# Performance work log

Measured on AMD Instinct MI355X. Metric: run time of the kernel, lower is better.

Reference implementation:

```python
import jax, jax.numpy as jnp
import numpy as np

B, C, H, W = 2, 128, 64, 64
HEADS, DHEAD = 4, 32
K = 7           # kernel_size (dilation = 1)
GROUPS = 32
EPS = 1e-5
DA = HEADS * DHEAD


def setup_inputs() -> dict:
    key = jax.random.key(0)
    ks = jax.random.split(key, 8)
    s = lambda k, sh: jax.random.normal(k, sh, jnp.float32) * 0.02
    return {
        "x": jax.random.normal(ks[0], (B, C, H, W), jnp.float32),
        "gn_weight": jnp.ones((C,), jnp.float32),
        "gn_bias": jnp.zeros((C,), jnp.float32),
        "wq": s(ks[1], (DA, C)), "bq": jnp.zeros((DA,), jnp.float32),
        "wk": s(ks[2], (DA, C)), "bk": jnp.zeros((DA,), jnp.float32),
        "wv": s(ks[3], (DA, C)), "bv": jnp.zeros((DA,), jnp.float32),
        "wo": s(ks[4], (C, DA)), "bo": jnp.zeros((C,), jnp.float32),
        "rpb": s(ks[5], (HEADS, 2 * K - 1, 2 * K - 1)),
    }


def _win_starts(L):
    # NATTEN window start: clamp so the k-window stays in-bounds
    return jnp.clip(jnp.arange(L) - K // 2, 0, L - K)


def _pb_starts(L):
    # NATTEN relative-position-bias start index along one axis
    idx = jnp.arange(L)
    ns = K // 2
    return ns + jnp.maximum(ns - idx, 0) + jnp.minimum(L - idx - 1 - ns, 0)


def reference(x, gn_weight, gn_bias, wq, bq, wk, bk, wv, bv, wo, bo, rpb):
    Bn, Cn, Hn, Wn = x.shape
    # GroupNorm (biased variance, like torch)
    xg = x.reshape(Bn, GROUPS, -1)
    mu = xg.mean(-1, keepdims=True)
    var = xg.var(-1, keepdims=True)
    xg = (xg - mu) * jax.lax.rsqrt(var + EPS)
    xn = xg.reshape(Bn, Cn, Hn, Wn) * gn_weight[:, None, None] + gn_bias[:, None, None]

    def proj(w, b):
        # 1x1 conv == channel matmul; -> (B, heads, H, W, d)
        y = jnp.einsum('bchw,oc->bohw', xn, w) + b[:, None, None]
        return y.reshape(Bn, HEADS, DHEAD, Hn, Wn).transpose(0, 1, 3, 4, 2)

    q = proj(wq, bq) * (DHEAD ** -0.5)
    k = proj(wk, bk)
    v = proj(wv, bv)

    off = jnp.arange(K)
    ih = _win_starts(Hn)[:, None] + off        # (H, K) neighbor rows
    iw = _win_starts(Wn)[:, None] + off        # (W, K) neighbor cols
    # gathered windows: (B, heads, H, W, K, K, d)
    kw = k[:, :, ih[:, None, :, None], iw[None, :, None, :], :]
    vw = v[:, :, ih[:, None, :, None], iw[None, :, None, :], :]

    bh = _pb_starts(Hn)[:, None] + off         # (H, K)
    bw = _pb_starts(Wn)[:, None] + off         # (W, K)
    bias = rpb[:, bh[:, None, :, None], bw[None, :, None, :]]  # (heads, H, W, K, K)

    attn = jnp.einsum('nhpqd,nhpqijd->nhpqij', q, kw) + bias[None]
    attn = jax.nn.softmax(attn.reshape(Bn, HEADS, Hn, Wn, K * K), axis=-1)
    attn = attn.reshape(Bn, HEADS, Hn, Wn, K, K)
    out = jnp.einsum('nhpqij,nhpqijd->nhpqd', attn, vw)  # (B, heads, H, W, d)
    # faithful to the torch code: raw reshape (B,heads,H,W,d)->(B,H,W,heads*d)
    xo = out.reshape(Bn, Hn, Wn, HEADS * DHEAD).transpose(0, 3, 1, 2)
    return jnp.einsum('bchw,oc->bohw', xo, wo) + bo[:, None, None]
```

## Files before the change

### kernel.cpp

```cpp
#include <hip/hip_runtime.h>

#define EPS 1e-5f

typedef short s8v __attribute__((ext_vector_type(8)));
typedef float f4v __attribute__((ext_vector_type(4)));

static __device__ inline short f2bf(float f) {
  return __builtin_bit_cast(short, (__bf16)f);
}

#define OFF_SP    0
#define OFF_S2P   256
#define OFF_WCB   512
#define OFF_BC    (OFF_WCB + 24576)
#define OFF_QB    (OFF_BC + 384)
#define OFF_KB    (OFF_QB + 524288)
#define OFF_VTB   (OFF_KB + 524288)
#define OFF_WOB   (OFF_VTB + 524288)

__global__ __launch_bounds__(256) void kP(
    const float* __restrict__ wq, const float* __restrict__ bq,
    const float* __restrict__ wk, const float* __restrict__ bk,
    const float* __restrict__ wv, const float* __restrict__ bv,
    const float* __restrict__ wo, const float* __restrict__ x,
    short* __restrict__ Wcb, float* __restrict__ bc,
    short* __restrict__ WoB, float* __restrict__ Spart, float* __restrict__ S2part) {
  int blk = blockIdx.x;
  int tid = threadIdx.x;
  if (blk < 64) {
    int t = blk * 256 + tid;
    const float qs = 0.17677669529663687f;
    Wcb[t]         = f2bf(wq[t] * qs);
    Wcb[16384 + t] = f2bf(wk[t]);
    Wcb[32768 + t] = f2bf(wv[t]);
    WoB[t]         = f2bf(wo[t]);
    if (t < 128) {
      bc[t]       = bq[t] * qs;
      bc[128 + t] = bk[t];
      bc[256 + t] = bv[t];
    }
  } else {
    int idx = blk - 64;
    int g = idx >> 2, part = idx & 3;
    const float4* xp = (const float4*)(x + (size_t)g * 16384 + part * 4096);
    float s = 0.f, s2 = 0.f;
    #pragma unroll
    for (int i = 0; i < 4; i++) {
      float4 v = xp[tid + i * 256];
      s  += v.x + v.y + v.z + v.w;
      s2 += v.x*v.x + v.y*v.y + v.z*v.z + v.w*v.w;
    }
    #pragma unroll
    for (int o = 32; o; o >>= 1) {
      s  += __shfl_down(s, o, 64);
      s2 += __shfl_down(s2, o, 64);
    }
    __shared__ float ls[4], ls2[4];
    int wid = tid >> 6, lane = tid & 63;
    if (!lane) { ls[wid] = s; ls2[wid] = s2; }
    __syncthreads();
    if (tid == 0) {
      float S = 0.f, S2 = 0.f;
      #pragma unroll
      for (int i = 0; i < 4; i++) { S += ls[i]; S2 += ls2[i]; }
      Spart[idx]  = S;
      S2part[idx] = S2;
    }
  }
}

__global__ __launch_bounds__(256) void k2_qkv(
    const float* __restrict__ x,
    const float* __restrict__ Spart, const float* __restrict__ S2part,
    const float* __restrict__ gw, const float* __restrict__ gb,
    const short* __restrict__ Wcb, const float* __restrict__ bc,
    short* __restrict__ qb, short* __restrict__ kb, short* __restrict__ vtb) {
  __shared__ short xn[64][136];
  __shared__ short WL[192][136];
  __shared__ float bcs[192];
  __shared__ float sm_s[128], sm_t[128];
  int bid    = blockIdx.x;
  int ptile  = bid >> 1, nslice = bid & 1;
  int b      = ptile >> 6;
  int pbase  = (ptile & 63) * 64;
  int nbase  = nslice * 192;
  int tid    = threadIdx.x;
  int w      = __builtin_amdgcn_readfirstlane(tid >> 6);
  int lane   = tid & 63;

  float va[16], vb[16];
  #pragma unroll
  for (int i = 0; i < 16; i++) {
    int c0 = (w + i * 4) * 2;
    va[i] = x[((size_t)(b * 128 + c0))     * 4096 + pbase + lane];
    vb[i] = x[((size_t)(b * 128 + c0 + 1)) * 4096 + pbase + lane];
  }
  if (tid < 128) {
    int c = tid, gi = (b * 32 + (c >> 2)) * 4;
    float S  = Spart[gi]  + Spart[gi + 1]  + Spart[gi + 2]  + Spart[gi + 3];
    float S2 = S2part[gi] + S2part[gi + 1] + S2part[gi + 2] + S2part[gi + 3];
    float mean = S * (1.f / 16384.f);
    float var  = S2 * (1.f / 16384.f) - mean * mean;
    float sv   = rsqrtf(var + EPS) * gw[c];
    sm_s[c] = sv;
    sm_t[c] = gb[c] - mean * sv;
  }
  #pragma unroll
  for (int i = 0; i < 12; i++) {
    int cc = tid + i * 256;
    int row = cc >> 4, c8 = (cc & 15) * 8;
    *(s8v*)&WL[row][c8] = *(const s8v*)&Wcb[(nbase + row) * 128 + c8];
  }
  if (tid < 192) bcs[tid] = bc[nbase + tid];
  __syncthreads();

  #pragma unroll
  for (int i = 0; i < 16; i++) {
    int c0 = (w + i * 4) * 2;
    ushort e0 = (ushort)f2bf(fmaf(va[i], sm_s[c0],     sm_t[c0]));
    ushort e1 = (ushort)f2bf(fmaf(vb[i], sm_s[c0 + 1], sm_t[c0 + 1]));
    *(uint*)&xn[lane][c0] = ((uint)e1 << 16) | e0;
  }
  __syncthreads();

  int l15 = lane & 15, kh = lane >> 4;
  f4v acc[12];
  #pragma unroll
  for (int nt = 0; nt < 12; nt++) acc[nt] = (f4v){0.f, 0.f, 0.f, 0.f};
  #pragma unroll
  for (int ks = 0; ks < 4; ks++) {
    s8v a = *(s8v*)&xn[w * 16 + l15][ks * 32 + kh * 8];
    #pragma unroll
    for (int nt = 0; nt < 12; nt++) {
      s8v wf = *(s8v*)&WL[nt * 16 + l15][ks * 32 + kh * 8];
      if (nbase + nt * 16 < 256)
        acc[nt] = __builtin_amdgcn_mfma_f32_16x16x32_bf16(wf, a, acc[nt], 0, 0, 0);
      else
        acc[nt] = __builtin_amdgcn_mfma_f32_16x16x32_bf16(a, wf, acc[nt], 0, 0, 0);
    }
  }
  #pragma unroll
  for (int nt = 0; nt < 12; nt++) {
    if (nbase + nt * 16 < 256) {
      int ob  = nt * 16 + kh * 4;
      int o0i = nbase + ob;
      int hd  = (o0i & 127) >> 5, d0 = o0i & 31;
      int bh2 = b * 4 + hd;
      int px  = pbase + w * 16 + l15;
      short* dst = (o0i >> 7) ? kb : qb;
      ushort e0 = (ushort)f2bf(acc[nt][0] + bcs[ob + 0]);
      ushort e1 = (ushort)f2bf(acc[nt][1] + bcs[ob + 1]);
      ushort e2 = (ushort)f2bf(acc[nt][2] + bcs[ob + 2]);
      ushort e3 = (ushort)f2bf(acc[nt][3] + bcs[ob + 3]);
      uint2 pk = make_uint2(((uint)e1 << 16) | e0, ((uint)e3 << 16) | e2);
      *(uint2*)&dst[((size_t)bh2 * 4096 + px) * 32 + d0] = pk;
    } else {
      int o   = nbase + nt * 16 + l15;
      int hd  = (o & 127) >> 5, d = o & 31;
      int bh2 = b * 4 + hd;
      int px0 = pbase + w * 16 + kh * 4;
      float bias = bcs[nt * 16 + l15];
      ushort s0 = (ushort)f2bf(acc[nt][0] + bias);
      ushort s1 = (ushort)f2bf(acc[nt][1] + bias);
      ushort s2 = (ushort)f2bf(acc[nt][2] + bias);
      ushort s3 = (ushort)f2bf(acc[nt][3] + bias);
      uint2 pk2 = make_uint2(((uint)s1 << 16) | s0, ((uint)s3 << 16) | s2);
      *(uint2*)&vtb[((size_t)bh2 * 32 + d) * 4096 + px0] = pk2;
    }
  }
}

__global__ __launch_bounds__(512) void k3_attn_proj(
    const short* __restrict__ qb, const short* __restrict__ kb, const short* __restrict__ vtb,
    const float* __restrict__ rpb, const short* __restrict__ WoB,
    const float* __restrict__ bo, float* __restrict__ out) {
  __shared__ ushort K_s[8][64][32];
  __shared__ ushort VT_s[8][32][68];
  __shared__ ushort P_s[8][16][40];
  __shared__ ushort Wo_s[128][136];
  __shared__ ushort tile_s[2][16][136];
  __shared__ float  rpb_s[176];

  int lb    = blockIdx.x;
  int bh    = lb & 7;
  int chunk = lb >> 3;
  int y0    = chunk * 2;
  int head  = bh & 3, b = bh >> 2;
  int tid   = threadIdx.x;
  int w     = __builtin_amdgcn_readfirstlane(tid >> 6);
  int lane  = tid & 63, l15 = lane & 15, kh = lane >> 4;
  int wsub  = w & 3, rsel = w >> 2;
  int y     = y0 + rsel;
  int ys0   = min(max(y0 - 3, 0), 57);
  int ysoff = min(max(y - 3, 0), 57) - ys0;

  {
    const size_t kbase = (size_t)bh * 4096 * 32;
    #pragma unroll
    for (int i = 0; i < 4; i++) {
      int cc = tid + i * 512;
      int row = cc >> 8, rem = cc & 255;
      int col = rem >> 2, ch8 = (rem & 3) * 8;
      int yr = min(ys0 + row, 63);
      *(s8v*)&K_s[row][col][ch8] = *(const s8v*)&kb[kbase + (size_t)(yr * 64 + col) * 32 + ch8];
    }
  }
  {
    const size_t vbase = (size_t)bh * 32 * 4096;
    #pragma unroll
    for (int i = 0; i < 4; i++) {
      int cc = tid + i * 512;
      int row = cc >> 8, rem = cc & 255;
      int d = rem >> 3, c8 = (rem & 7) * 8;
      int yr = min(ys0 + row, 63);
      *(s8v*)&VT_s[row][d][c8] = *(const s8v*)&vtb[vbase + (size_t)d * 4096 + yr * 64 + c8];
    }
  }
  #pragma unroll
  for (int i = 0; i < 4; i++) {
    int cc = tid + i * 512;
    int row = cc >> 4, c8 = (cc & 15) * 8;
    *(s8v*)&Wo_s[row][c8] = *(const s8v*)&WoB[row * 128 + c8];
  }
  if (tid < 169) rpb_s[tid] = rpb[head * 169 + tid];
  __syncthreads();

  int c0  = wsub * 8 + (wsub >> 1) * 8;
  int xq  = wsub * 16 + l15;
  int xs  = min(max(xq - 3, 0), 57);
  int pbw = 3 + max(3 - xq, 0) + min(60 - xq, 0);
  int pbh = 3 + max(3 - y, 0) + min(60 - y, 0);

  s8v qf = *(const s8v*)&qb[((size_t)bh * 4096 + y * 64 + xq) * 32 + kh * 8];

  int   bidx[8];
  float badd[8];
  #pragma unroll
  for (int j = 0; j < 8; ++j) {
    int cc = (j >> 2) * 16 + kh * 4 + (j & 3);
    int dx = c0 + cc - xs;
    bool valid = (dx >= 0) && (dx < 7);
    bidx[j] = pbw + min(max(dx, 0), 6);
    badd[j] = valid ? 0.f : -1e30f;
  }

  const f4v zero = {0.f, 0.f, 0.f, 0.f};
  f4v o0 = zero, o1 = zero;
  float ssum = 0.f;

  #pragma unroll
  for (int row = 0; row < 7; ++row) {
    int kr = ysoff + row;
    s8v ka0 = *(s8v*)&K_s[kr][c0 + l15][kh * 8];
    s8v ka1 = *(s8v*)&K_s[kr][c0 + 16 + l15][kh * 8];
    f4v lg0 = __builtin_amdgcn_mfma_f32_16x16x32_bf16(ka0, qf, zero, 0, 0, 0);
    f4v lg1 = __builtin_amdgcn_mfma_f32_16x16x32_bf16(ka1, qf, zero, 0, 0, 0);
    int rbase = (pbh + row) * 13;
    float p[8];
    #pragma unroll
    for (int j = 0; j < 4; ++j) {
      p[j]     = __expf(lg0[j] + rpb_s[rbase + bidx[j]]     + badd[j]);
      p[j + 4] = __expf(lg1[j] + rpb_s[rbase + bidx[j + 4]] + badd[j + 4]);
      ssum += p[j] + p[j + 4];
    }
    uint u0 = ((uint)(ushort)f2bf(p[1]) << 16) | (ushort)f2bf(p[0]);
    uint u1 = ((uint)(ushort)f2bf(p[3]) << 16) | (ushort)f2bf(p[2]);
    uint u2 = ((uint)(ushort)f2bf(p[5]) << 16) | (ushort)f2bf(p[4]);
    uint u3 = ((uint)(ushort)f2bf(p[7]) << 16) | (ushort)f2bf(p[6]);
    *(uint2*)&P_s[w][l15][kh * 4]      = make_uint2(u0, u1);
    *(uint2*)&P_s[w][l15][16 + kh * 4] = make_uint2(u2, u3);
    s8v pa  = *(s8v*)&P_s[w][l15][kh * 8];
    s8v vt0 = *(s8v*)&VT_s[kr][l15][c0 + kh * 8];
    s8v vt1 = *(s8v*)&VT_s[kr][16 + l15][c0 + kh * 8];
    o0 = __builtin_amdgcn_mfma_f32_16x16x32_bf16(pa, vt0, o0, 0, 0, 0);
    o1 = __builtin_amdgcn_mfma_f32_16x16x32_bf16(pa, vt1, o1, 0, 0, 0);
  }

  ssum += __shfl_xor(ssum, 16, 64);
  ssum += __shfl_xor(ssum, 32, 64);

  {
    int col = wsub * 4 + kh;
    #pragma unroll
    for (int r = 0; r < 4; ++r) {
      float sq = __builtin_bit_cast(float,
          __builtin_amdgcn_ds_bpermute((kh * 4 + r) << 2, __builtin_bit_cast(int, ssum)));
      float inv = 1.f / sq;
      tile_s[rsel][col][r * 32 + l15]      = (ushort)f2bf(o0[r] * inv);
      tile_s[rsel][col][r * 32 + 16 + l15] = (ushort)f2bf(o1[r] * inv);
    }
  }
  __syncthreads();

  f4v acc2[2];
  acc2[0] = zero; acc2[1] = zero;
  #pragma unroll
  for (int ks = 0; ks < 4; ks++) {
    s8v a = *(s8v*)&tile_s[rsel][l15][ks * 32 + kh * 8];
    #pragma unroll
    for (int nt = 0; nt < 2; nt++) {
      s8v bf = *(s8v*)&Wo_s[wsub * 32 + nt * 16 + l15][ks * 32 + kh * 8];
      acc2[nt] = __builtin_amdgcn_mfma_f32_16x16x32_bf16(a, bf, acc2[nt], 0, 0, 0);
    }
  }
  int pxg = (head * 16 + (y >> 2)) * 64 + ((y & 3) << 4);
  #pragma unroll
  for (int nt = 0; nt < 2; nt++) {
    int o = wsub * 32 + nt * 16 + l15;
    float bias = bo[o];
    float4 val = make_float4(acc2[nt][0] + bias, acc2[nt][1] + bias,
                             acc2[nt][2] + bias, acc2[nt][3] + bias);
    *(float4*)&out[((size_t)b * 128 + o) * 4096 + pxg + kh * 4] = val;
  }
}

extern "C" void kernel_launch(void* const* d_in, const int* in_sizes, int n_in,
                              void* d_out, int out_size, void* d_ws, size_t ws_size,
                              hipStream_t stream) {
  (void)in_sizes; (void)n_in; (void)out_size; (void)ws_size;
  const float* x   = (const float*)d_in[0];
  const float* gw  = (const float*)d_in[1];
  const float* gb  = (const float*)d_in[2];
  const float* wq  = (const float*)d_in[3];
  const float* bq  = (const float*)d_in[4];
  const float* wk  = (const float*)d_in[5];
  const float* bk  = (const float*)d_in[6];
  const float* wv  = (const float*)d_in[7];
  const float* bv  = (const float*)d_in[8];
  const float* wo  = (const float*)d_in[9];
  const float* bo  = (const float*)d_in[10];
  const float* rpb = (const float*)d_in[11];
  float* ws     = (float*)d_ws;
  float* Spart  = ws + OFF_SP;
  float* S2part = ws + OFF_S2P;
  short* Wcb    = (short*)(ws + OFF_WCB);
  float* bc     = ws + OFF_BC;
  short* qb     = (short*)(ws + OFF_QB);
  short* kb     = (short*)(ws + OFF_KB);
  short* vtb    = (short*)(ws + OFF_VTB);
  short* WoB    = (short*)(ws + OFF_WOB);
  float* out    = (float*)d_out;

  hipLaunchKernelGGL(kP, dim3(320), dim3(256), 0, stream,
                     wq, bq, wk, bk, wv, bv, wo, x, Wcb, bc, WoB, Spart, S2part);
  hipLaunchKernelGGL(k2_qkv, dim3(256), dim3(256), 0, stream,
                     x, Spart, S2part, gw, gb, Wcb, bc, qb, kb, vtb);
  hipLaunchKernelGGL(k3_attn_proj, dim3(256), dim3(512), 0, stream,
                     qb, kb, vtb, rpb, WoB, bo, out);
}
```

Before: 26.96 us.

## Split attention kernel into one-row blocks and keep Wo fragments in registers

The attention+projection kernel now uses 512 blocks of 256 threads, each handling a single query row instead of two. This cuts the staged K/V tile from 8 rows to 7 and drops the shared-memory Wo copy: each wave loads its Wo fragments directly into registers. The P buffer is reused as the output tile after an added barrier. All QK logits are computed up front before the softmax/PV loop to give the scheduler more independent MFMA work. Shared memory per block shrinks so more blocks can be resident, at the cost of more register pressure and redundant K/V and Wo loads across blocks.

New measurement: 28.70 us. 6.5% more time.

```diff
diff --git a/kernel.cpp b/kernel.cpp
--- a/kernel.cpp
+++ b/kernel.cpp
@@ -170,68 +170,62 @@
   }
 }
 
-__global__ __launch_bounds__(512) void k3_attn_proj(
+__global__ __launch_bounds__(256, 2) void k3_attn_proj(
     const short* __restrict__ qb, const short* __restrict__ kb, const short* __restrict__ vtb,
     const float* __restrict__ rpb, const short* __restrict__ WoB,
     const float* __restrict__ bo, float* __restrict__ out) {
-  __shared__ ushort K_s[8][64][32];
-  __shared__ ushort VT_s[8][32][68];
-  __shared__ ushort P_s[8][16][40];
-  __shared__ ushort Wo_s[128][136];
-  __shared__ ushort tile_s[2][16][136];
+  __shared__ ushort K_s[7][64][32];
+  __shared__ ushort VT_s[7][32][68];
+  __shared__ ushort PT_s[4][16][36];
   __shared__ float  rpb_s[176];
 
-  int lb    = blockIdx.x;
-  int bh    = lb & 7;
-  int chunk = lb >> 3;
-  int y0    = chunk * 2;
-  int head  = bh & 3, b = bh >> 2;
-  int tid   = threadIdx.x;
-  int w     = __builtin_amdgcn_readfirstlane(tid >> 6);
-  int lane  = tid & 63, l15 = lane & 15, kh = lane >> 4;
-  int wsub  = w & 3, rsel = w >> 2;
-  int y     = y0 + rsel;
-  int ys0   = min(max(y0 - 3, 0), 57);
-  int ysoff = min(max(y - 3, 0), 57) - ys0;
+  int lb   = blockIdx.x;
+  int bh   = lb & 7;
+  int y    = lb >> 3;
+  int head = bh & 3, b = bh >> 2;
+  int tid  = threadIdx.x;
+  int w    = __builtin_amdgcn_readfirstlane(tid >> 6);
+  int lane = tid & 63, l15 = lane & 15, kh = lane >> 4;
+  int ys   = min(max(y - 3, 0), 57);
+
+  int c0  = w * 8 + (w >> 1) * 8;
+  int xq  = w * 16 + l15;
+  s8v wof[2][4];
+  #pragma unroll
+  for (int nt = 0; nt < 2; nt++)
+    #pragma unroll
+    for (int ks = 0; ks < 4; ks++)
+      wof[nt][ks] = *(const s8v*)&WoB[(w * 32 + nt * 16 + l15) * 128 + ks * 32 + kh * 8];
+  s8v qf = *(const s8v*)&qb[((size_t)bh * 4096 + y * 64 + xq) * 32 + kh * 8];
 
   {
     const size_t kbase = (size_t)bh * 4096 * 32;
     #pragma unroll
-    for (int i = 0; i < 4; i++) {
-      int cc = tid + i * 512;
+    for (int i = 0; i < 7; i++) {
+      int cc = tid + i * 256;
       int row = cc >> 8, rem = cc & 255;
       int col = rem >> 2, ch8 = (rem & 3) * 8;
-      int yr = min(ys0 + row, 63);
-      *(s8v*)&K_s[row][col][ch8] = *(const s8v*)&kb[kbase + (size_t)(yr * 64 + col) * 32 + ch8];
+      *(s8v*)&K_s[row][col][ch8] =
+          *(const s8v*)&kb[kbase + (size_t)((ys + row) * 64 + col) * 32 + ch8];
     }
   }
   {
     const size_t vbase = (size_t)bh * 32 * 4096;
     #pragma unroll
-    for (int i = 0; i < 4; i++) {
-      int cc = tid + i * 512;
+    for (int i = 0; i < 7; i++) {
+      int cc = tid + i * 256;
       int row = cc >> 8, rem = cc & 255;
       int d = rem >> 3, c8 = (rem & 7) * 8;
-      int yr = min(ys0 + row, 63);
-      *(s8v*)&VT_s[row][d][c8] = *(const s8v*)&vtb[vbase + (size_t)d * 4096 + yr * 64 + c8];
-    }
-  }
-  #pragma unroll
-  for (int i = 0; i < 4; i++) {
-    int cc = tid + i * 512;
-    int row = cc >> 4, c8 = (cc & 15) * 8;
-    *(s8v*)&Wo_s[row][c8] = *(const s8v*)&WoB[row * 128 + c8];
+      *(s8v*)&VT_s[row][d][c8] =
+          *(const s8v*)&vtb[vbase + (size_t)d * 4096 + (ys + row) * 64 + c8];
+    }
   }
   if (tid < 169) rpb_s[tid] = rpb[head * 169 + tid];
   __syncthreads();
 
-  int c0  = wsub * 8 + (wsub >> 1) * 8;
-  int xq  = wsub * 16 + l15;
   int xs  = min(max(xq - 3, 0), 57);
   int pbw = 3 + max(3 - xq, 0) + min(60 - xq, 0);
   int pbh = 3 + max(3 - y, 0) + min(60 - y, 0);
-
-  s8v qf = *(const s8v*)&qb[((size_t)bh * 4096 + y * 64 + xq) * 32 + kh * 8];
 
   int   bidx[8];
   float badd[8];
@@ -245,33 +239,37 @@
   }
 
   const f4v zero = {0.f, 0.f, 0.f, 0.f};
+
+  f4v lg0[7], lg1[7];
+  #pragma unroll
+  for (int row = 0; row < 7; ++row) {
+    s8v ka0 = *(s8v*)&K_s[row][c0 + l15][kh * 8];
+    s8v ka1 = *(s8v*)&K_s[row][c0 + 16 + l15][kh * 8];
+    lg0[row] = __builtin_amdgcn_mfma_f32_16x16x32_bf16(ka0, qf, zero, 0, 0, 0);
+    lg1[row] = __builtin_amdgcn_mfma_f32_16x16x32_bf16(ka1, qf, zero, 0, 0, 0);
+  }
+
   f4v o0 = zero, o1 = zero;
   float ssum = 0.f;
-
   #pragma unroll
   for (int row = 0; row < 7; ++row) {
-    int kr = ysoff + row;
-    s8v ka0 = *(s8v*)&K_s[kr][c0 + l15][kh * 8];
-    s8v ka1 = *(s8v*)&K_s[kr][c0 + 16 + l15][kh * 8];
-    f4v lg0 = __builtin_amdgcn_mfma_f32_16x16x32_bf16(ka0, qf, zero, 0, 0, 0);
-    f4v lg1 = __builtin_amdgcn_mfma_f32_16x16x32_bf16(ka1, qf, zero, 0, 0, 0);
     int rbase = (pbh + row) * 13;
     float p[8];
     #pragma unroll
     for (int j = 0; j < 4; ++j) {
-      p[j]     = __expf(lg0[j] + rpb_s[rbase + bidx[j]]     + badd[j]);
-      p[j + 4] = __expf(lg1[j] + rpb_s[rbase + bidx[j + 4]] + badd[j + 4]);
+      p[j]     = __expf(lg0[row][j] + rpb_s[rbase + bidx[j]]     + badd[j]);
+      p[j + 4] = __expf(lg1[row][j] + rpb_s[rbase + bidx[j + 4]] + badd[j + 4]);
       ssum += p[j] + p[j + 4];
     }
     uint u0 = ((uint)(ushort)f2bf(p[1]) << 16) | (ushort)f2bf(p[0]);
     uint u1 = ((uint)(ushort)f2bf(p[3]) << 16) | (ushort)f2bf(p[2]);
     uint u2 = ((uint)(ushort)f2bf(p[5]) << 16) | (ushort)f2bf(p[4]);
     uint u3 = ((uint)(ushort)f2bf(p[7]) << 16) | (ushort)f2bf(p[6]);
-    *(uint2*)&P_s[w][l15][kh * 4]      = make_uint2(u0, u1);
-    *(uint2*)&P_s[w][l15][16 + kh * 4] = make_uint2(u2, u3);
-    s8v pa  = *(s8v*)&P_s[w][l15][kh * 8];
-    s8v vt0 = *(s8v*)&VT_s[kr][l15][c0 + kh * 8];
-    s8v vt1 = *(s8v*)&VT_s[kr][16 + l15][c0 + kh * 8];
+    *(uint2*)&PT_s[w][l15][kh * 4]      = make_uint2(u0, u1);
+    *(uint2*)&PT_s[w][l15][16 + kh * 4] = make_uint2(u2, u3);
+    s8v pa  = *(s8v*)&PT_s[w][l15][kh * 8];
+    s8v vt0 = *(s8v*)&VT_s[row][l15][c0 + kh * 8];
+    s8v vt1 = *(s8v*)&VT_s[row][16 + l15][c0 + kh * 8];
     o0 = __builtin_amdgcn_mfma_f32_16x16x32_bf16(pa, vt0, o0, 0, 0, 0);
     o1 = __builtin_amdgcn_mfma_f32_16x16x32_bf16(pa, vt1, o1, 0, 0, 0);
   }
@@ -279,15 +277,18 @@
   ssum += __shfl_xor(ssum, 16, 64);
   ssum += __shfl_xor(ssum, 32, 64);
 
+  __syncthreads();
+
+  ushort* tile = (ushort*)PT_s;
   {
-    int col = wsub * 4 + kh;
+    int col = w * 4 + kh;
     #pragma unroll
     for (int r = 0; r < 4; ++r) {
       float sq = __builtin_bit_cast(float,
           __builtin_amdgcn_ds_bpermute((kh * 4 + r) << 2, __builtin_bit_cast(int, ssum)));
       float inv = 1.f / sq;
-      tile_s[rsel][col][r * 32 + l15]      = (ushort)f2bf(o0[r] * inv);
-      tile_s[rsel][col][r * 32 + 16 + l15] = (ushort)f2bf(o1[r] * inv);
+      tile[col * 132 + r * 32 + l15]      = (ushort)f2bf(o0[r] * inv);
+      tile[col * 132 + r * 32 + 16 + l15] = (ushort)f2bf(o1[r] * inv);
     }
   }
   __syncthreads();
@@ -296,17 +297,15 @@
   acc2[0] = zero; acc2[1] = zero;
   #pragma unroll
   for (int ks = 0; ks < 4; ks++) {
-    s8v a = *(s8v*)&tile_s[rsel][l15][ks * 32 + kh * 8];
-    #pragma unroll
-    for (int nt = 0; nt < 2; nt++) {
-      s8v bf = *(s8v*)&Wo_s[wsub * 32 + nt * 16 + l15][ks * 32 + kh * 8];
-      acc2[nt] = __builtin_amdgcn_mfma_f32_16x16x32_bf16(a, bf, acc2[nt], 0, 0, 0);
-    }
+    s8v a = *(s8v*)&tile[l15 * 132 + ks * 32 + kh * 8];
+    #pragma unroll
+    for (int nt = 0; nt < 2; nt++)
+      acc2[nt] = __builtin_amdgcn_mfma_f32_16x16x32_bf16(a, wof[nt][ks], acc2[nt], 0, 0, 0);
   }
   int pxg = (head * 16 + (y >> 2)) * 64 + ((y & 3) << 4);
   #pragma unroll
   for (int nt = 0; nt < 2; nt++) {
-    int o = wsub * 32 + nt * 16 + l15;
+    int o = w * 32 + nt * 16 + l15;
     float bias = bo[o];
     float4 val = make_float4(acc2[nt][0] + bias, acc2[nt][1] + bias,
                              acc2[nt][2] + bias, acc2[nt][3] + bias);
@@ -345,6 +344,6 @@
                      wq, bq, wk, bk, wv, bv, wo, x, Wcb, bc, WoB, Spart, S2part);
   hipLaunchKernelGGL(k2_qkv, dim3(256), dim3(256), 0, stream,
                      x, Spart, S2part, gw, gb, Wcb, bc, qb, kb, vtb);
-  hipLaunchKernelGGL(k3_attn_proj, dim3(256), dim3(512), 0, stream,
+  hipLaunchKernelGGL(k3_attn_proj, dim3(512), dim3(256), 0, stream,
                      qb, kb, vtb, rpb, WoB, bo, out);
 }
```
